# Kernel tuning notes

Hardware: AMD Instinct MI355X
Metric: run time of the kernel (lower is better)

Reference implementation:

```python
import jax, jax.numpy as jnp
import numpy as np
from jax import lax

BN_EPS = 1e-5

def _conv1d_same(x, w):
    # x: [N, 1, C], w: [1, 1, k] with k odd -> SAME padding along channel axis
    k = w.shape[-1]
    return lax.conv_general_dilated(x, w, window_strides=(1,),
                                    padding=[(k // 2, k // 2)],
                                    dimension_numbers=('NCH', 'OIH', 'NCH'))

def setup_inputs() -> dict:
    key = jax.random.key(0)
    ks = jax.random.split(key, 6)
    B, C, H, W = 4, 64, 64, 64
    kk = 3  # kernel size from in_dim=64: t=int(abs(log2(64)+1)/2)=3 (odd)
    x = jax.random.normal(ks[0], (B, C, H, W), dtype=jnp.float32)
    q_w = jax.random.normal(ks[1], (1, 1, kk), dtype=jnp.float32) * 0.5
    k_w = jax.random.normal(ks[2], (1, 1, kk), dtype=jnp.float32) * 0.5
    v_w = jax.random.normal(ks[3], (C, C), dtype=jnp.float32) * (1.0 / np.sqrt(C))
    v_b = jnp.zeros((C,), dtype=jnp.float32)
    gamma = jax.random.uniform(ks[4], (1,), dtype=jnp.float32, minval=0.5, maxval=1.5)
    bn_w = jnp.ones((C,), dtype=jnp.float32)
    bn_b = jnp.zeros((C,), dtype=jnp.float32)
    return {"x": x, "q_w": q_w, "k_w": k_w, "v_w": v_w, "v_b": v_b,
            "gamma": gamma, "bn_w": bn_w, "bn_b": bn_b}

def reference(x, q_w, k_w, v_w, v_b, gamma, bn_w, bn_b):
    B, C, H, W = x.shape
    N = H * W
    # conv1d Q/K projections over the channel axis, per spatial position
    xp = x.reshape(B, C, N).transpose(0, 2, 1).reshape(B * N, 1, C)
    q = _conv1d_same(xp, q_w).reshape(B, N, C)   # proj_query: [B, HW, C]
    k = _conv1d_same(xp, k_w).reshape(B, N, C)   # proj_key (pre-permute)
    energy = jnp.einsum('bnc,bmc->bnm', q, k)    # [B, HW, HW]
    attn = jax.nn.softmax(energy, axis=-1)
    # 1x1 value conv
    v = jnp.einsum('oc,bchw->bohw', v_w, x) + v_b[None, :, None, None]
    vv = v.reshape(B, C, N)
    # bmm(value, attention^T)
    out = jnp.einsum('bcm,bnm->bcn', vv, attn).reshape(B, C, H, W)
    y = gamma[0] * out
    # BatchNorm2d, training mode (batch statistics, biased variance)
    mean = jnp.mean(y, axis=(0, 2, 3), keepdims=True)
    var = jnp.var(y, axis=(0, 2, 3), keepdims=True)
    y = (y - mean) * lax.rsqrt(var + BN_EPS)
    y = y * bn_w[None, :, None, None] + bn_b[None, :, None, None]
    return y + x
```

## Files before the change

### kernel.cpp

```cpp
#include <hip/hip_runtime.h>
#include <stdint.h>

using f16 = _Float16;

typedef _Float16 f16x8 __attribute__((ext_vector_type(8)));
typedef _Float16 f16x4 __attribute__((ext_vector_type(4)));
typedef float f32x4 __attribute__((ext_vector_type(4)));

#define LOG2E 1.44269504088896340736f

__device__ __forceinline__ f16 f2h(float f) { return (f16)f; }

#if __has_builtin(__builtin_amdgcn_exp2f)
__device__ __forceinline__ float fexp2(float x) { return __builtin_amdgcn_exp2f(x); }
#else
__device__ __forceinline__ float fexp2(float x) { return exp2f(x); }
#endif

typedef __attribute__((address_space(1))) const uint32_t gu32;
typedef __attribute__((address_space(3))) uint32_t lu32;

__device__ __forceinline__ void dma16(const void* g, void* l) {
  __builtin_amdgcn_global_load_lds((gu32*)g, (lu32*)l, 16, 0, 0);
}

__device__ __forceinline__ f16x8 cvt8(const float* p) {
  const float4 a = *(const float4*)p;
  const float4 b = *(const float4*)(p + 4);
  f16x8 r;
  r[0] = (f16)a.x; r[1] = (f16)a.y; r[2] = (f16)a.z; r[3] = (f16)a.w;
  r[4] = (f16)b.x; r[5] = (f16)b.y; r[6] = (f16)b.z; r[7] = (f16)b.w;
  return r;
}


__global__ __launch_bounds__(256, 2) void pam_pre(
    const float* __restrict__ x, const float* __restrict__ qw,
    const float* __restrict__ kw, const float* __restrict__ vw,
    const float* __restrict__ vb,
    f16* __restrict__ qa, f16* __restrict__ ka2, f16* __restrict__ va3,
    float* __restrict__ gz)
{
  __shared__ alignas(16) f16 xt[16 * 72];
  const int tid = threadIdx.x;
  const int b = blockIdx.x >> 8;
  const int n0 = (blockIdx.x & 255) << 4;
  const int lane = tid & 63;
  const int wv = tid >> 6;
  const int quad = lane >> 4, l15 = lane & 15;

  if (blockIdx.x == 0 && tid < 128) gz[tid] = 0.f;

  {
    const int c = tid >> 2;
    const int j0 = (tid & 3) << 2;
    const float4 v0 = *(const float4*)(x + ((size_t)(b * 64 + c) << 12) + n0 + j0);
    xt[(j0 + 0) * 72 + c] = f2h(v0.x);
    xt[(j0 + 1) * 72 + c] = f2h(v0.y);
    xt[(j0 + 2) * 72 + c] = f2h(v0.z);
    xt[(j0 + 3) * 72 + c] = f2h(v0.w);
  }
  __syncthreads();

  const float qw0 = qw[0], qw1 = qw[1], qw2 = qw[2];
  const float kw0 = kw[0], kw1 = kw[1], kw2 = kw[2];
  for (int p = 0; p < 4; ++p) {
    const int c = lane;
    const int jr = (p << 2) + wv;
    const int n = n0 + jr;
    const float xm = (c > 0) ? (float)xt[jr * 72 + c - 1] : 0.f;
    const float x0 = (float)xt[jr * 72 + c];
    const float xp = (c < 63) ? (float)xt[jr * 72 + c + 1] : 0.f;
    const float qv = (qw0 * xm + qw1 * x0 + qw2 * xp) * LOG2E;
    const float kv = kw0 * xm + kw1 * x0 + kw2 * xp;
    qa[((size_t)((b << 12) + n) << 6) + c] = f2h(qv);
    ka2[((size_t)(b * 8 + (c >> 3)) << 15) + (n << 3) + (c & 7)] = f2h(kv);
  }

  {
    const f16x8 a0 = cvt8(vw + (wv * 16 + l15) * 64 + quad * 8);
    const f16x8 a1 = cvt8(vw + (wv * 16 + l15) * 64 + quad * 8 + 32);
    const f16x8 b0 = *(const f16x8*)&xt[l15 * 72 + quad * 8];
    const f16x8 b1 = *(const f16x8*)&xt[l15 * 72 + quad * 8 + 32];
    f32x4 z = {0.f, 0.f, 0.f, 0.f};
    z = __builtin_amdgcn_mfma_f32_16x16x32_f16(a0, b0, z, 0, 0, 0);
    z = __builtin_amdgcn_mfma_f32_16x16x32_f16(a1, b1, z, 0, 0, 0);
    const int cobase = wv * 16 + quad * 4;
    for (int r = 0; r < 4; ++r) {
      const int co = cobase + r;
      const int n = n0 + l15;
      const float val = z[r] + vb[co];
      va3[(((size_t)(b * 512 + (n >> 3))) << 9) + (co << 3) + (n & 7)] = f2h(val);
    }
  }
}

__global__ __launch_bounds__(512, 2) void pam_attn(
    const f16* __restrict__ qa, const f16* __restrict__ ka2,
    const f16* __restrict__ va3, const float* __restrict__ gam,
    float* __restrict__ y0, float* __restrict__ gs1, float* __restrict__ gs2)
{
  __shared__ alignas(16) f16 kbuf[2][8192];
  __shared__ alignas(16) f16 vbuf[2][8192];
  __shared__ float ldsO[32 * 65];
  __shared__ float ldsM[4][32], ldsL[4][32], ldsMg[32], ldsInv[32];

  const int tid = threadIdx.x;
  const int wv = tid >> 6, lane = tid & 63;
  const int quad = lane >> 4, l15 = lane & 15;
  const int ks = wv & 3, qh = wv >> 2;
  const int b = blockIdx.x & 3;
  const int qb = blockIdx.x >> 2;
  const int qb0 = qb << 5;
  const int phase = qb & 31;

  for (int i = tid; i < 32 * 65; i += 512) ldsO[i] = 0.f;

  const int bn = b << 12;
  f16x8 bq0, bq1;
  {
    const int q = qb0 + qh * 16 + l15;
    const f16* qp = qa + ((size_t)(bn + q) << 6) + quad * 8;
    bq0 = *(const f16x8*)qp;
    bq1 = *(const f16x8*)(qp + 32);
  }

  const f16* kg0 = ka2 + (((size_t)(b * 8 + wv)) << 15) + (lane << 3);
  const f16* vg0 = va3 + ((size_t)b << 18) + (wv << 10) + (lane << 3);

  f32x4 o[4] = {};
  float m = -1e30f, lp = 0.f;

  dma16(kg0 + ((size_t)phase << 10),       kbuf[0] + (wv << 10));
  dma16(kg0 + ((size_t)phase << 10) + 512, kbuf[0] + (wv << 10) + 512);
  dma16(vg0 + ((size_t)phase << 13),       vbuf[0] + (wv << 10));
  dma16(vg0 + ((size_t)phase << 13) + 512, vbuf[0] + (wv << 10) + 512);
  __syncthreads();

  const int kperm = (ks << 5) + (((l15 >> 2) << 3) | (l15 & 3));
  const int koff0 = kperm << 3;
  const int koff1 = (kperm + 4) << 3;
  const int vbase = ((ks * 4 + quad) << 9) + (l15 << 3);

#pragma unroll 1
  for (int kt = 0; kt < 32; ++kt) {
    const int cur = kt & 1;
    {
      const int tn = (kt + 1 + phase) & 31;
      f16* kd = kbuf[cur ^ 1] + (wv << 10);
      f16* vd = vbuf[cur ^ 1] + (wv << 10);
      dma16(kg0 + ((size_t)tn << 10),       kd);
      dma16(kg0 + ((size_t)tn << 10) + 512, kd + 512);
      dma16(vg0 + ((size_t)tn << 13),       vd);
      dma16(vg0 + ((size_t)tn << 13) + 512, vd + 512);
    }

    const f16* kc = kbuf[cur];
    const f16* vc = vbuf[cur];
    const f16x8 ak00 = *(const f16x8*)(kc + (quad << 10) + koff0);
    const f16x8 ak01 = *(const f16x8*)(kc + ((4 + quad) << 10) + koff0);
    const f16x8 ak10 = *(const f16x8*)(kc + (quad << 10) + koff1);
    const f16x8 ak11 = *(const f16x8*)(kc + ((4 + quad) << 10) + koff1);

    f32x4 z0, z1;
    {
      f32x4 z = {0.f, 0.f, 0.f, 0.f};
      z = __builtin_amdgcn_mfma_f32_16x16x32_f16(ak00, bq0, z, 0, 0, 0);
      z0 = __builtin_amdgcn_mfma_f32_16x16x32_f16(ak01, bq1, z, 0, 0, 0);
    }
    {
      f32x4 z = {0.f, 0.f, 0.f, 0.f};
      z = __builtin_amdgcn_mfma_f32_16x16x32_f16(ak10, bq0, z, 0, 0, 0);
      s1_label:
      z1 = __builtin_amdgcn_mfma_f32_16x16x32_f16(ak11, bq1, z, 0, 0, 0);
    }

    float tmax = fmaxf(fmaxf(fmaxf(z0[0], z0[1]), fmaxf(z0[2], z0[3])),
                       fmaxf(fmaxf(z1[0], z1[1]), fmaxf(z1[2], z1[3])));
    tmax = fmaxf(tmax, __shfl_xor(tmax, 16, 64));
    tmax = fmaxf(tmax, __shfl_xor(tmax, 32, 64));
    const bool need = !__all(tmax <= m + 8.f);
    const float mn = need ? fmaxf(m, tmax) : m;

    const float p0 = fexp2(z0[0] - mn);
    const float p1 = fexp2(z0[1] - mn);
    const float p2 = fexp2(z0[2] - mn);
    const float p3 = fexp2(z0[3] - mn);
    const float p4 = fexp2(z1[0] - mn);
    const float p5 = fexp2(z1[1] - mn);
    const float p6 = fexp2(z1[2] - mn);
    const float p7 = fexp2(z1[3] - mn);
    const float ts = ((p0 + p1) + (p2 + p3)) + ((p4 + p5) + (p6 + p7));

    f16x8 pa;
    pa[0] = f2h(p0); pa[1] = f2h(p1); pa[2] = f2h(p2); pa[3] = f2h(p3);
    pa[4] = f2h(p4); pa[5] = f2h(p5); pa[6] = f2h(p6); pa[7] = f2h(p7);

    if (need) {
      const float al = fexp2(m - mn);
      lp = lp * al + ts;
      m = mn;
#pragma unroll
      for (int ct = 0; ct < 4; ++ct)
        for (int r = 0; r < 4; ++r) o[ct][r] *= al;
    } else {
      lp += ts;
    }

#pragma unroll
    for (int ct = 0; ct < 4; ++ct) {
      const f16x8 av = *(const f16x8*)(vc + vbase + ct * 128);
      o[ct] = __builtin_amdgcn_mfma_f32_16x16x32_f16(av, pa, o[ct], 0, 0, 0);
    }
    __syncthreads();
  }

  {
    float v = lp;
    v += __shfl_xor(v, 16, 64);
    v += __shfl_xor(v, 32, 64);
    if (quad == 0) {
      ldsM[ks][qh * 16 + l15] = m;
      ldsL[ks][qh * 16 + l15] = v;
    }
  }
  __syncthreads();

  if (tid < 32) {
    const float M = fmaxf(fmaxf(ldsM[0][tid], ldsM[1][tid]),
                          fmaxf(ldsM[2][tid], ldsM[3][tid]));
    const float lt = ldsL[0][tid] * fexp2(ldsM[0][tid] - M) +
                     ldsL[1][tid] * fexp2(ldsM[1][tid] - M) +
                     ldsL[2][tid] * fexp2(ldsM[2][tid] - M) +
                     ldsL[3][tid] * fexp2(ldsM[3][tid] - M);
    ldsMg[tid] = M;
    ldsInv[tid] = 1.f / lt;
  }
  __syncthreads();

  {
    const int q = qh * 16 + l15;
    const float sc = fexp2(m - ldsMg[q]);
#pragma unroll
    for (int ct = 0; ct < 4; ++ct)
      for (int r = 0; r < 4; ++r)
        atomicAdd(&ldsO[q * 65 + ct * 16 + quad * 4 + r], o[ct][r] * sc);
  }
  __syncthreads();

  const float g = gam[0];
  {
    const int c = tid >> 3;
    const int q0 = (tid & 7) << 2;
    float4 v4;
    float* vp = &v4.x;
    float s1 = 0.f, s2 = 0.f;
    for (int r = 0; r < 4; ++r) {
      const float val = g * ldsO[(q0 + r) * 65 + c] * ldsInv[q0 + r];
      vp[r] = val; s1 += val; s2 += val * val;
    }
    *(float4*)(y0 + ((size_t)(b * 64 + c) << 12) + qb0 + q0) = v4;
    s1 += __shfl_xor(s1, 1, 64);
    s2 += __shfl_xor(s2, 1, 64);
    s1 += __shfl_xor(s1, 2, 64);
    s2 += __shfl_xor(s2, 2, 64);
    s1 += __shfl_xor(s1, 4, 64);
    s2 += __shfl_xor(s2, 4, 64);
    if ((tid & 7) == 0) {
      atomicAdd(&gs1[c], s1);
      atomicAdd(&gs2[c], s2);
    }
  }
}

__global__ __launch_bounds__(256, 2) void pam_apply(
    const float* __restrict__ y0, const float* __restrict__ x,
    const float* __restrict__ gs1, const float* __restrict__ gs2,
    const float* __restrict__ bnw, const float* __restrict__ bnb,
    float* __restrict__ out)
{
  const int i = (blockIdx.x * 256 + threadIdx.x) << 2;
  const int c = (i >> 12) & 63;
  const float inv_n = 1.f / 16384.f;
  const float mean = gs1[c] * inv_n;
  const float var = fmaxf(gs2[c] * inv_n - mean * mean, 0.f);
  const float sc = bnw[c] * rsqrtf(var + 1e-5f);
  const float sh = bnb[c] - mean * sc;
  const float4 y = *(const float4*)(y0 + i);
  const float4 xv = *(const float4*)(x + i);
  float4 r;
  r.x = y.x * sc + sh + xv.x;
  r.y = y.y * sc + sh + xv.y;
  r.z = y.z * sc + sh + xv.z;
  r.w = y.w * sc + sh + xv.w;
  *(float4*)(out + i) = r;
}

extern "C" void kernel_launch(void* const* d_in, const int* in_sizes, int n_in,
                              void* d_out, int out_size, void* d_ws, size_t ws_size,
                              hipStream_t stream)
{
  (void)in_sizes; (void)n_in; (void)out_size; (void)ws_size;
  const float* x   = (const float*)d_in[0];
  const float* qw  = (const float*)d_in[1];
  const float* kw  = (const float*)d_in[2];
  const float* vw  = (const float*)d_in[3];
  const float* vb  = (const float*)d_in[4];
  const float* gam = (const float*)d_in[5];
  const float* bnw = (const float*)d_in[6];
  const float* bnb = (const float*)d_in[7];

  char* ws = (char*)d_ws;
  f16*   qa  = (f16*)(ws);
  f16*   ka2 = (f16*)(ws + (2u << 20));
  f16*   va3 = (f16*)(ws + (4u << 20));
  float* y0  = (float*)(ws + (6u << 20));
  float* gs1 = (float*)(ws + (10u << 20));
  float* gs2 = (float*)(ws + (10u << 20) + 256);

  pam_pre  <<<1024, 256, 0, stream>>>(x, qw, kw, vw, vb, qa, ka2, va3, gs1);
  pam_attn <<<512, 512, 0, stream>>>(qa, ka2, va3, gam, y0, gs1, gs2);
  pam_apply<<<1024, 256, 0, stream>>>(y0, x, gs1, gs2, bnw, bnb, (float*)d_out);
}
```

Measured before the change: 149.7 us.

## Widen attention blocks to 64 queries and 1024 threads with swizzled K layout

The attention kernel now processes 64 queries per block using 16 waves, with 8 key splits and two query sub-tiles per wave. Each K/V tile loaded into LDS is therefore reused across twice as many queries, halving the grid and the total K/V traffic. Tiles are twice as large (128 keys) and staged in 128KB of dynamic LDS, which is aliased for the output reduction. The K layout written by the pre-kernel is XOR-swizzled to avoid LDS bank conflicts on the new read pattern. The cost is higher LDS and register pressure per block and only 256 blocks to spread across the GPU.

```diff
diff --git a/kernel.cpp b/kernel.cpp
--- a/kernel.cpp
+++ b/kernel.cpp
@@ -74,7 +74,8 @@
     const float qv = (qw0 * xm + qw1 * x0 + qw2 * xp) * LOG2E;
     const float kv = kw0 * xm + kw1 * x0 + kw2 * xp;
     qa[((size_t)((b << 12) + n) << 6) + c] = f2h(qv);
-    ka2[((size_t)(b * 8 + (c >> 3)) << 15) + (n << 3) + (c & 7)] = f2h(kv);
+    const int np = n ^ ((((n >> 3) & 1) << 2) | ((n >> 4) & 1));
+    ka2[((size_t)(b * 8 + (c >> 3)) << 15) + (np << 3) + (c & 7)] = f2h(kv);
   }
 
   {
@@ -95,166 +96,208 @@
   }
 }
 
-__global__ __launch_bounds__(512, 2) void pam_attn(
+__global__ __launch_bounds__(1024, 4) void pam_attn(
     const f16* __restrict__ qa, const f16* __restrict__ ka2,
     const f16* __restrict__ va3, const float* __restrict__ gam,
     float* __restrict__ y0, float* __restrict__ gs1, float* __restrict__ gs2)
 {
-  __shared__ alignas(16) f16 kbuf[2][8192];
-  __shared__ alignas(16) f16 vbuf[2][8192];
-  __shared__ float ldsO[32 * 65];
-  __shared__ float ldsM[4][32], ldsL[4][32], ldsMg[32], ldsInv[32];
+  extern __shared__ char smem[];
+  f16* const kbase = (f16*)smem;
+  f16* const vbase2 = (f16*)(smem + 65536);
+  float* const ldsO = (float*)smem;
+  __shared__ float ldsM[8][64], ldsL[8][64], ldsMg[64], ldsInv[64];
 
   const int tid = threadIdx.x;
   const int wv = tid >> 6, lane = tid & 63;
   const int quad = lane >> 4, l15 = lane & 15;
-  const int ks = wv & 3, qh = wv >> 2;
-  const int b = blockIdx.x & 3;
-  const int qb = blockIdx.x >> 2;
-  const int qb0 = qb << 5;
-  const int phase = qb & 31;
-
-  for (int i = tid; i < 32 * 65; i += 512) ldsO[i] = 0.f;
+  const int ks = wv & 7, qh = wv >> 3;
+  const int slot = (int)blockIdx.x & 7;
+  const int b = slot >> 1;
+  const int qb = (((int)blockIdx.x >> 3) << 1) | (slot & 1);
+  const int qb0 = qb << 6;
+  const int phase = qb & 15;
 
   const int bn = b << 12;
-  f16x8 bq0, bq1;
-  {
-    const int q = qb0 + qh * 16 + l15;
-    const f16* qp = qa + ((size_t)(bn + q) << 6) + quad * 8;
-    bq0 = *(const f16x8*)qp;
-    bq1 = *(const f16x8*)(qp + 32);
-  }
-
-  const f16* kg0 = ka2 + (((size_t)(b * 8 + wv)) << 15) + (lane << 3);
+  f16x8 bq00, bq01, bq10, bq11;
+  {
+    const f16* qp0 = qa + ((size_t)(bn + qb0 + qh * 32 + l15) << 6) + quad * 8;
+    bq00 = *(const f16x8*)qp0;
+    bq01 = *(const f16x8*)(qp0 + 32);
+    const f16* qp1 = qp0 + (16 << 6);
+    bq10 = *(const f16x8*)qp1;
+    bq11 = *(const f16x8*)(qp1 + 32);
+  }
+
+  const f16* kg0 = ka2 + (((size_t)(b * 8 + (wv >> 1))) << 15)
+                 + ((wv & 1) << 10) + (lane << 3);
   const f16* vg0 = va3 + ((size_t)b << 18) + (wv << 10) + (lane << 3);
 
-  f32x4 o[4] = {};
-  float m = -1e30f, lp = 0.f;
-
-  dma16(kg0 + ((size_t)phase << 10),       kbuf[0] + (wv << 10));
-  dma16(kg0 + ((size_t)phase << 10) + 512, kbuf[0] + (wv << 10) + 512);
-  dma16(vg0 + ((size_t)phase << 13),       vbuf[0] + (wv << 10));
-  dma16(vg0 + ((size_t)phase << 13) + 512, vbuf[0] + (wv << 10) + 512);
-  __syncthreads();
-
-  const int kperm = (ks << 5) + (((l15 >> 2) << 3) | (l15 & 3));
-  const int koff0 = kperm << 3;
-  const int koff1 = (kperm + 4) << 3;
+  f32x4 o0[4] = {}, o1[4] = {};
+  float m0 = -1e30f, lp0 = 0.f, m1 = -1e30f, lp1 = 0.f;
+
+  dma16(kg0 + ((size_t)phase << 11),       kbase + (wv << 10));
+  dma16(kg0 + ((size_t)phase << 11) + 512, kbase + (wv << 10) + 512);
+  dma16(vg0 + ((size_t)phase << 14),       vbase2 + (wv << 10));
+  dma16(vg0 + ((size_t)phase << 14) + 512, vbase2 + (wv << 10) + 512);
+  __syncthreads();
+
+  const int u = l15 >> 2;
+  const int xm = ((u & 1) << 2) | (u >> 1);
+  const int pos0 = (ks << 5) + (u << 3) + (l15 & 3);
+  const int koff0 = (pos0 ^ xm) << 3;
+  const int koff1 = koff0 ^ 32;
   const int vbase = ((ks * 4 + quad) << 9) + (l15 << 3);
 
 #pragma unroll 1
-  for (int kt = 0; kt < 32; ++kt) {
+  for (int kt = 0; kt < 16; ++kt) {
     const int cur = kt & 1;
-    {
-      const int tn = (kt + 1 + phase) & 31;
-      f16* kd = kbuf[cur ^ 1] + (wv << 10);
-      f16* vd = vbuf[cur ^ 1] + (wv << 10);
-      dma16(kg0 + ((size_t)tn << 10),       kd);
-      dma16(kg0 + ((size_t)tn << 10) + 512, kd + 512);
-      dma16(vg0 + ((size_t)tn << 13),       vd);
-      dma16(vg0 + ((size_t)tn << 13) + 512, vd + 512);
-    }
-
-    const f16* kc = kbuf[cur];
-    const f16* vc = vbuf[cur];
-    const f16x8 ak00 = *(const f16x8*)(kc + (quad << 10) + koff0);
-    const f16x8 ak01 = *(const f16x8*)(kc + ((4 + quad) << 10) + koff0);
-    const f16x8 ak10 = *(const f16x8*)(kc + (quad << 10) + koff1);
-    const f16x8 ak11 = *(const f16x8*)(kc + ((4 + quad) << 10) + koff1);
-
-    f32x4 z0, z1;
+    if (kt < 15) {
+      const int tn = (kt + 1 + phase) & 15;
+      f16* kd = kbase + ((cur ^ 1) << 14) + (wv << 10);
+      f16* vd = vbase2 + ((cur ^ 1) << 14) + (wv << 10);
+      dma16(kg0 + ((size_t)tn << 11),       kd);
+      dma16(kg0 + ((size_t)tn << 11) + 512, kd + 512);
+      dma16(vg0 + ((size_t)tn << 14),       vd);
+      dma16(vg0 + ((size_t)tn << 14) + 512, vd + 512);
+    }
+
+    const f16* kc = kbase + (cur << 14);
+    const f16* vc = vbase2 + (cur << 14);
+    const f16x8 ak00 = *(const f16x8*)(kc + (quad << 11) + koff0);
+    const f16x8 ak01 = *(const f16x8*)(kc + ((4 + quad) << 11) + koff0);
+    const f16x8 ak10 = *(const f16x8*)(kc + (quad << 11) + koff1);
+    const f16x8 ak11 = *(const f16x8*)(kc + ((4 + quad) << 11) + koff1);
+
+    f32x4 za0, zb0, za1, zb1;
     {
       f32x4 z = {0.f, 0.f, 0.f, 0.f};
-      z = __builtin_amdgcn_mfma_f32_16x16x32_f16(ak00, bq0, z, 0, 0, 0);
-      z0 = __builtin_amdgcn_mfma_f32_16x16x32_f16(ak01, bq1, z, 0, 0, 0);
+      z = __builtin_amdgcn_mfma_f32_16x16x32_f16(ak00, bq00, z, 0, 0, 0);
+      za0 = __builtin_amdgcn_mfma_f32_16x16x32_f16(ak01, bq01, z, 0, 0, 0);
     }
     {
       f32x4 z = {0.f, 0.f, 0.f, 0.f};
-      z = __builtin_amdgcn_mfma_f32_16x16x32_f16(ak10, bq0, z, 0, 0, 0);
-      s1_label:
-      z1 = __builtin_amdgcn_mfma_f32_16x16x32_f16(ak11, bq1, z, 0, 0, 0);
-    }
-
-    float tmax = fmaxf(fmaxf(fmaxf(z0[0], z0[1]), fmaxf(z0[2], z0[3])),
-                       fmaxf(fmaxf(z1[0], z1[1]), fmaxf(z1[2], z1[3])));
-    tmax = fmaxf(tmax, __shfl_xor(tmax, 16, 64));
-    tmax = fmaxf(tmax, __shfl_xor(tmax, 32, 64));
-    const bool need = !__all(tmax <= m + 8.f);
-    const float mn = need ? fmaxf(m, tmax) : m;
-
-    const float p0 = fexp2(z0[0] - mn);
-    const float p1 = fexp2(z0[1] - mn);
-    const float p2 = fexp2(z0[2] - mn);
-    const float p3 = fexp2(z0[3] - mn);
-    const float p4 = fexp2(z1[0] - mn);
-    const float p5 = fexp2(z1[1] - mn);
-    const float p6 = fexp2(z1[2] - mn);
-    const float p7 = fexp2(z1[3] - mn);
-    const float ts = ((p0 + p1) + (p2 + p3)) + ((p4 + p5) + (p6 + p7));
-
-    f16x8 pa;
-    pa[0] = f2h(p0); pa[1] = f2h(p1); pa[2] = f2h(p2); pa[3] = f2h(p3);
-    pa[4] = f2h(p4); pa[5] = f2h(p5); pa[6] = f2h(p6); pa[7] = f2h(p7);
-
-    if (need) {
-      const float al = fexp2(m - mn);
-      lp = lp * al + ts;
-      m = mn;
-#pragma unroll
-      for (int ct = 0; ct < 4; ++ct)
-        for (int r = 0; r < 4; ++r) o[ct][r] *= al;
-    } else {
-      lp += ts;
+      z = __builtin_amdgcn_mfma_f32_16x16x32_f16(ak10, bq00, z, 0, 0, 0);
+      zb0 = __builtin_amdgcn_mfma_f32_16x16x32_f16(ak11, bq01, z, 0, 0, 0);
+    }
+    {
+      f32x4 z = {0.f, 0.f, 0.f, 0.f};
+      z = __builtin_amdgcn_mfma_f32_16x16x32_f16(ak00, bq10, z, 0, 0, 0);
+      za1 = __builtin_amdgcn_mfma_f32_16x16x32_f16(ak01, bq11, z, 0, 0, 0);
+    }
+    {
+      f32x4 z = {0.f, 0.f, 0.f, 0.f};
+      z = __builtin_amdgcn_mfma_f32_16x16x32_f16(ak10, bq10, z, 0, 0, 0);
+      zb1 = __builtin_amdgcn_mfma_f32_16x16x32_f16(ak11, bq11, z, 0, 0, 0);
+    }
+
+    f16x8 pa0, pa1;
+    {
+      float tmax = fmaxf(fmaxf(fmaxf(za0[0], za0[1]), fmaxf(za0[2], za0[3])),
+                         fmaxf(fmaxf(zb0[0], zb0[1]), fmaxf(zb0[2], zb0[3])));
+      tmax = fmaxf(tmax, __shfl_xor(tmax, 16, 64));
+      tmax = fmaxf(tmax, __shfl_xor(tmax, 32, 64));
+      const bool need = !__all(tmax <= m0 + 8.f);
+      const float mn = need ? fmaxf(m0, tmax) : m0;
+      const float p0 = fexp2(za0[0] - mn), p1 = fexp2(za0[1] - mn);
+      const float p2 = fexp2(za0[2] - mn), p3 = fexp2(za0[3] - mn);
+      const float p4 = fexp2(zb0[0] - mn), p5 = fexp2(zb0[1] - mn);
+      const float p6 = fexp2(zb0[2] - mn), p7 = fexp2(zb0[3] - mn);
+      const float ts = ((p0 + p1) + (p2 + p3)) + ((p4 + p5) + (p6 + p7));
+      pa0[0] = f2h(p0); pa0[1] = f2h(p1); pa0[2] = f2h(p2); pa0[3] = f2h(p3);
+      pa0[4] = f2h(p4); pa0[5] = f2h(p5); pa0[6] = f2h(p6); pa0[7] = f2h(p7);
+      if (need) {
+        const float al = fexp2(m0 - mn);
+        lp0 = lp0 * al + ts;
+        m0 = mn;
+#pragma unroll
+        for (int ct = 0; ct < 4; ++ct)
+          for (int r = 0; r < 4; ++r) o0[ct][r] *= al;
+      } else {
+        lp0 += ts;
+      }
+    }
+    {
+      float tmax = fmaxf(fmaxf(fmaxf(za1[0], za1[1]), fmaxf(za1[2], za1[3])),
+                         fmaxf(fmaxf(zb1[0], zb1[1]), fmaxf(zb1[2], zb1[3])));
+      tmax = fmaxf(tmax, __shfl_xor(tmax, 16, 64));
+      tmax = fmaxf(tmax, __shfl_xor(tmax, 32, 64));
+      const bool need = !__all(tmax <= m1 + 8.f);
+      const float mn = need ? fmaxf(m1, tmax) : m1;
+      const float p0 = fexp2(za1[0] - mn), p1 = fexp2(za1[1] - mn);
+      const float p2 = fexp2(za1[2] - mn), p3 = fexp2(za1[3] - mn);
+      const float p4 = fexp2(zb1[0] - mn), p5 = fexp2(zb1[1] - mn);
+      const float p6 = fexp2(zb1[2] - mn), p7 = fexp2(zb1[3] - mn);
+      const float ts = ((p0 + p1) + (p2 + p3)) + ((p4 + p5) + (p6 + p7));
+      pa1[0] = f2h(p0); pa1[1] = f2h(p1); pa1[2] = f2h(p2); pa1[3] = f2h(p3);
+      pa1[4] = f2h(p4); pa1[5] = f2h(p5); pa1[6] = f2h(p6); pa1[7] = f2h(p7);
+      if (need) {
+        const float al = fexp2(m1 - mn);
+        lp1 = lp1 * al + ts;
+        m1 = mn;
+#pragma unroll
+        for (int ct = 0; ct < 4; ++ct)
+          for (int r = 0; r < 4; ++r) o1[ct][r] *= al;
+      } else {
+        lp1 += ts;
+      }
     }
 
 #pragma unroll
     for (int ct = 0; ct < 4; ++ct) {
       const f16x8 av = *(const f16x8*)(vc + vbase + ct * 128);
-      o[ct] = __builtin_amdgcn_mfma_f32_16x16x32_f16(av, pa, o[ct], 0, 0, 0);
+      o0[ct] = __builtin_amdgcn_mfma_f32_16x16x32_f16(av, pa0, o0[ct], 0, 0, 0);
+      o1[ct] = __builtin_amdgcn_mfma_f32_16x16x32_f16(av, pa1, o1[ct], 0, 0, 0);
     }
     __syncthreads();
   }
 
-  {
-    float v = lp;
-    v += __shfl_xor(v, 16, 64);
-    v += __shfl_xor(v, 32, 64);
-    if (quad == 0) {
-      ldsM[ks][qh * 16 + l15] = m;
-      ldsL[ks][qh * 16 + l15] = v;
-    }
-  }
-  __syncthreads();
-
-  if (tid < 32) {
-    const float M = fmaxf(fmaxf(ldsM[0][tid], ldsM[1][tid]),
-                          fmaxf(ldsM[2][tid], ldsM[3][tid]));
-    const float lt = ldsL[0][tid] * fexp2(ldsM[0][tid] - M) +
-                     ldsL[1][tid] * fexp2(ldsM[1][tid] - M) +
-                     ldsL[2][tid] * fexp2(ldsM[2][tid] - M) +
-                     ldsL[3][tid] * fexp2(ldsM[3][tid] - M);
+  lp0 += __shfl_xor(lp0, 16, 64);
+  lp0 += __shfl_xor(lp0, 32, 64);
+  lp1 += __shfl_xor(lp1, 16, 64);
+  lp1 += __shfl_xor(lp1, 32, 64);
+  if (quad == 0) {
+    ldsM[ks][qh * 32 + l15] = m0;
+    ldsL[ks][qh * 32 + l15] = lp0;
+    ldsM[ks][qh * 32 + 16 + l15] = m1;
+    ldsL[ks][qh * 32 + 16 + l15] = lp1;
+  }
+  __syncthreads();
+
+  for (int i = tid; i < 64 * 65; i += 1024) ldsO[i] = 0.f;
+  if (tid < 64) {
+    float M = ldsM[0][tid];
+#pragma unroll
+    for (int k = 1; k < 8; ++k) M = fmaxf(M, ldsM[k][tid]);
+    float lt = 0.f;
+#pragma unroll
+    for (int k = 0; k < 8; ++k) lt += ldsL[k][tid] * fexp2(ldsM[k][tid] - M);
     ldsMg[tid] = M;
     ldsInv[tid] = 1.f / lt;
   }
   __syncthreads();
 
   {
-    const int q = qh * 16 + l15;
-    const float sc = fexp2(m - ldsMg[q]);
+    const int q0i = qh * 32 + l15, q1i = q0i + 16;
+    const float sc0 = fexp2(m0 - ldsMg[q0i]);
+    const float sc1 = fexp2(m1 - ldsMg[q1i]);
 #pragma unroll
     for (int ct = 0; ct < 4; ++ct)
-      for (int r = 0; r < 4; ++r)
-        atomicAdd(&ldsO[q * 65 + ct * 16 + quad * 4 + r], o[ct][r] * sc);
+      for (int r = 0; r < 4; ++r) {
+        const int c = ct * 16 + quad * 4 + r;
+        atomicAdd(&ldsO[q0i * 65 + c], o0[ct][r] * sc0);
+        atomicAdd(&ldsO[q1i * 65 + c], o1[ct][r] * sc1);
+      }
   }
   __syncthreads();
 
   const float g = gam[0];
   {
-    const int c = tid >> 3;
-    const int q0 = (tid & 7) << 2;
+    const int c = tid >> 4;
+    const int q0 = (tid & 15) << 2;
     float4 v4;
     float* vp = &v4.x;
     float s1 = 0.f, s2 = 0.f;
+#pragma unroll
     for (int r = 0; r < 4; ++r) {
       const float val = g * ldsO[(q0 + r) * 65 + c] * ldsInv[q0 + r];
       vp[r] = val; s1 += val; s2 += val * val;
@@ -266,7 +309,9 @@
     s2 += __shfl_xor(s2, 2, 64);
     s1 += __shfl_xor(s1, 4, 64);
     s2 += __shfl_xor(s2, 4, 64);
-    if ((tid & 7) == 0) {
+    s1 += __shfl_xor(s1, 8, 64);
+    s2 += __shfl_xor(s2, 8, 64);
+    if ((tid & 15) == 0) {
       atomicAdd(&gs1[c], s1);
       atomicAdd(&gs2[c], s2);
     }
@@ -318,7 +363,14 @@
   float* gs1 = (float*)(ws + (10u << 20));
   float* gs2 = (float*)(ws + (10u << 20) + 256);
 
+  static bool lds_init = false;
+  if (!lds_init) {
+    (void)hipFuncSetAttribute((const void*)pam_attn,
+                              hipFuncAttributeMaxDynamicSharedMemorySize, 131072);
+    lds_init = true;
+  }
+
   pam_pre  <<<1024, 256, 0, stream>>>(x, qw, kw, vw, vb, qa, ka2, va3, gs1);
-  pam_attn <<<512, 512, 0, stream>>>(qa, ka2, va3, gam, y0, gs1, gs2);
+  pam_attn <<<256, 1024, 131072, stream>>>(qa, ka2, va3, gam, y0, gs1, gs2);
   pam_apply<<<1024, 256, 0, stream>>>(y0, x, gs1, gs2, bnw, bnb, (float*)d_out);
 }
```

Measured after the change: 176.6 us. 17.9% more time.

## Use 4-slot LDS ring with 64-key tiles and lighter barriers in attention

Applied to the files above, without the earlier changes.

Splits the key loop into 64 smaller tiles of 64 keys each and streams K/V into a 4-slot dynamic-LDS ring that prefetches two tiles ahead. The full __syncthreads is replaced by an explicit vmcnt wait plus s_barrier, so only the oldest loads are drained. The PV product switches to 16x16x16 MFMA with f16x4 operands. The output accumulation buffer now aliases the K region of the ring. The aim is to hide global-to-LDS latency and shrink per-iteration stalls, at the cost of twice as many loop iterations and softmax reductions, and the aliasing must not race with in-flight DMA.

```diff
diff --git a/kernel.cpp b/kernel.cpp
--- a/kernel.cpp
+++ b/kernel.cpp
@@ -100,9 +100,10 @@
     const f16* __restrict__ va3, const float* __restrict__ gam,
     float* __restrict__ y0, float* __restrict__ gs1, float* __restrict__ gs2)
 {
-  __shared__ alignas(16) f16 kbuf[2][8192];
-  __shared__ alignas(16) f16 vbuf[2][8192];
-  __shared__ float ldsO[32 * 65];
+  extern __shared__ char smem[];
+  f16* const kbase = (f16*)smem;
+  f16* const vbase = (f16*)(smem + 32768);
+  float* const ldsO = (float*)smem;
   __shared__ float ldsM[4][32], ldsL[4][32], ldsMg[32], ldsInv[32];
 
   const int tid = threadIdx.x;
@@ -112,9 +113,7 @@
   const int b = blockIdx.x & 3;
   const int qb = blockIdx.x >> 2;
   const int qb0 = qb << 5;
-  const int phase = qb & 31;
-
-  for (int i = tid; i < 32 * 65; i += 512) ldsO[i] = 0.f;
+  const int phase = qb & 63;
 
   const int bn = b << 12;
   f16x8 bq0, bq1;
@@ -126,75 +125,61 @@
   }
 
   const f16* kg0 = ka2 + (((size_t)(b * 8 + wv)) << 15) + (lane << 3);
-  const f16* vg0 = va3 + ((size_t)b << 18) + (wv << 10) + (lane << 3);
+  const f16* vg0 = va3 + ((size_t)b << 18) + (wv << 9) + (lane << 3);
 
   f32x4 o[4] = {};
   float m = -1e30f, lp = 0.f;
 
-  dma16(kg0 + ((size_t)phase << 10),       kbuf[0] + (wv << 10));
-  dma16(kg0 + ((size_t)phase << 10) + 512, kbuf[0] + (wv << 10) + 512);
-  dma16(vg0 + ((size_t)phase << 13),       vbuf[0] + (wv << 10));
-  dma16(vg0 + ((size_t)phase << 13) + 512, vbuf[0] + (wv << 10) + 512);
-  __syncthreads();
-
-  const int kperm = (ks << 5) + (((l15 >> 2) << 3) | (l15 & 3));
-  const int koff0 = kperm << 3;
-  const int koff1 = (kperm + 4) << 3;
-  const int vbase = ((ks * 4 + quad) << 9) + (l15 << 3);
+  {
+    const int g0 = phase;
+    const int g1 = (1 + phase) & 63;
+    dma16(kg0 + ((size_t)g0 << 9),  kbase + (wv << 9));
+    dma16(vg0 + ((size_t)g0 << 12), vbase + (wv << 9));
+    dma16(kg0 + ((size_t)g1 << 9),  kbase + 4096 + (wv << 9));
+    dma16(vg0 + ((size_t)g1 << 12), vbase + 4096 + (wv << 9));
+  }
+  asm volatile("s_waitcnt vmcnt(2)" ::: "memory");
+  __builtin_amdgcn_s_barrier();
+
+  const int krow = ((ks << 4) + l15) << 3;
+  const int vrow = ((ks * 2 + (quad >> 1)) << 9) + ((quad & 1) << 2);
 
 #pragma unroll 1
-  for (int kt = 0; kt < 32; ++kt) {
-    const int cur = kt & 1;
+  for (int kt = 0; kt < 64; ++kt) {
+    const int slot = kt & 3;
     {
-      const int tn = (kt + 1 + phase) & 31;
-      f16* kd = kbuf[cur ^ 1] + (wv << 10);
-      f16* vd = vbuf[cur ^ 1] + (wv << 10);
-      dma16(kg0 + ((size_t)tn << 10),       kd);
-      dma16(kg0 + ((size_t)tn << 10) + 512, kd + 512);
-      dma16(vg0 + ((size_t)tn << 13),       vd);
-      dma16(vg0 + ((size_t)tn << 13) + 512, vd + 512);
-    }
-
-    const f16* kc = kbuf[cur];
-    const f16* vc = vbuf[cur];
-    const f16x8 ak00 = *(const f16x8*)(kc + (quad << 10) + koff0);
-    const f16x8 ak01 = *(const f16x8*)(kc + ((4 + quad) << 10) + koff0);
-    const f16x8 ak10 = *(const f16x8*)(kc + (quad << 10) + koff1);
-    const f16x8 ak11 = *(const f16x8*)(kc + ((4 + quad) << 10) + koff1);
-
-    f32x4 z0, z1;
+      const int g = (kt + 2 + phase) & 63;
+      const int ps = ((kt + 2) & 3) << 12;
+      dma16(kg0 + ((size_t)g << 9),  kbase + ps + (wv << 9));
+      dma16(vg0 + ((size_t)g << 12), vbase + ps + (wv << 9));
+    }
+
+    const f16* kc = kbase + (slot << 12);
+    const f16* vc = vbase + (slot << 12);
+    const f16x8 ak0 = *(const f16x8*)(kc + (quad << 9) + krow);
+    const f16x8 ak1 = *(const f16x8*)(kc + ((4 + quad) << 9) + krow);
+
+    f32x4 z;
     {
-      f32x4 z = {0.f, 0.f, 0.f, 0.f};
-      z = __builtin_amdgcn_mfma_f32_16x16x32_f16(ak00, bq0, z, 0, 0, 0);
-      z0 = __builtin_amdgcn_mfma_f32_16x16x32_f16(ak01, bq1, z, 0, 0, 0);
-    }
-    {
-      f32x4 z = {0.f, 0.f, 0.f, 0.f};
-      z = __builtin_amdgcn_mfma_f32_16x16x32_f16(ak10, bq0, z, 0, 0, 0);
-      s1_label:
-      z1 = __builtin_amdgcn_mfma_f32_16x16x32_f16(ak11, bq1, z, 0, 0, 0);
-    }
-
-    float tmax = fmaxf(fmaxf(fmaxf(z0[0], z0[1]), fmaxf(z0[2], z0[3])),
-                       fmaxf(fmaxf(z1[0], z1[1]), fmaxf(z1[2], z1[3])));
+      f32x4 zz = {0.f, 0.f, 0.f, 0.f};
+      zz = __builtin_amdgcn_mfma_f32_16x16x32_f16(ak0, bq0, zz, 0, 0, 0);
+      z  = __builtin_amdgcn_mfma_f32_16x16x32_f16(ak1, bq1, zz, 0, 0, 0);
+    }
+
+    float tmax = fmaxf(fmaxf(z[0], z[1]), fmaxf(z[2], z[3]));
     tmax = fmaxf(tmax, __shfl_xor(tmax, 16, 64));
     tmax = fmaxf(tmax, __shfl_xor(tmax, 32, 64));
     const bool need = !__all(tmax <= m + 8.f);
     const float mn = need ? fmaxf(m, tmax) : m;
 
-    const float p0 = fexp2(z0[0] - mn);
-    const float p1 = fexp2(z0[1] - mn);
-    const float p2 = fexp2(z0[2] - mn);
-    const float p3 = fexp2(z0[3] - mn);
-    const float p4 = fexp2(z1[0] - mn);
-    const float p5 = fexp2(z1[1] - mn);
-    const float p6 = fexp2(z1[2] - mn);
-    const float p7 = fexp2(z1[3] - mn);
-    const float ts = ((p0 + p1) + (p2 + p3)) + ((p4 + p5) + (p6 + p7));
-
-    f16x8 pa;
+    const float p0 = fexp2(z[0] - mn);
+    const float p1 = fexp2(z[1] - mn);
+    const float p2 = fexp2(z[2] - mn);
+    const float p3 = fexp2(z[3] - mn);
+    const float ts = (p0 + p1) + (p2 + p3);
+
+    f16x4 pa;
     pa[0] = f2h(p0); pa[1] = f2h(p1); pa[2] = f2h(p2); pa[3] = f2h(p3);
-    pa[4] = f2h(p4); pa[5] = f2h(p5); pa[6] = f2h(p6); pa[7] = f2h(p7);
 
     if (need) {
       const float al = fexp2(m - mn);
@@ -209,23 +194,25 @@
 
 #pragma unroll
     for (int ct = 0; ct < 4; ++ct) {
-      const f16x8 av = *(const f16x8*)(vc + vbase + ct * 128);
-      o[ct] = __builtin_amdgcn_mfma_f32_16x16x32_f16(av, pa, o[ct], 0, 0, 0);
-    }
-    __syncthreads();
-  }
-
-  {
-    float v = lp;
-    v += __shfl_xor(v, 16, 64);
-    v += __shfl_xor(v, 32, 64);
-    if (quad == 0) {
-      ldsM[ks][qh * 16 + l15] = m;
-      ldsL[ks][qh * 16 + l15] = v;
-    }
+      const f16x4 av = *(const f16x4*)(vc + vrow + ((ct * 16 + l15) << 3));
+      o[ct] = __builtin_amdgcn_mfma_f32_16x16x16f16(av, pa, o[ct], 0, 0, 0);
+    }
+
+    asm volatile("s_waitcnt vmcnt(2)" ::: "memory");
+    __builtin_amdgcn_s_barrier();
+  }
+
+  asm volatile("s_waitcnt vmcnt(0)" ::: "memory");
+
+  lp += __shfl_xor(lp, 16, 64);
+  lp += __shfl_xor(lp, 32, 64);
+  if (quad == 0) {
+    ldsM[ks][qh * 16 + l15] = m;
+    ldsL[ks][qh * 16 + l15] = lp;
   }
   __syncthreads();
 
+  for (int i = tid; i < 32 * 65; i += 512) ldsO[i] = 0.f;
   if (tid < 32) {
     const float M = fmaxf(fmaxf(ldsM[0][tid], ldsM[1][tid]),
                           fmaxf(ldsM[2][tid], ldsM[3][tid]));
@@ -318,7 +305,14 @@
   float* gs1 = (float*)(ws + (10u << 20));
   float* gs2 = (float*)(ws + (10u << 20) + 256);
 
+  static bool lds_init = false;
+  if (!lds_init) {
+    (void)hipFuncSetAttribute((const void*)pam_attn,
+                              hipFuncAttributeMaxDynamicSharedMemorySize, 65536);
+    lds_init = true;
+  }
+
   pam_pre  <<<1024, 256, 0, stream>>>(x, qw, kw, vw, vb, qa, ka2, va3, gs1);
-  pam_attn <<<512, 512, 0, stream>>>(qa, ka2, va3, gam, y0, gs1, gs2);
+  pam_attn <<<512, 512, 65536, stream>>>(qa, ka2, va3, gam, y0, gs1, gs2);
   pam_apply<<<1024, 256, 0, stream>>>(y0, x, gs1, gs2, bnw, bnb, (float*)d_out);
 }
```

After: 161.1 us. +7.6%, slower.

## Widen pre-pass tiles, vectorize Q/K/V stores, and XOR-swizzle K layout

Applied to the files above, without the earlier changes.

The pre-pass kernel now handles 64 spatial positions per block instead of 16, cutting the grid from 1024 to 256 blocks. Q and K are computed eight channels per thread and written with 16-byte vector stores. The V projection is restructured so each wave reuses its x fragment across four output-channel tiles, writing f16x4 vectors. K is stored with an XOR permutation of position indices, and the attention kernel's K offsets are recomputed to match; the likely aim is to reduce LDS bank conflicts or simplify addressing. The pre-pass is a small share of total time, so most of the expected change comes from the K-read pattern in the attention loop.

```diff
diff --git a/kernel.cpp b/kernel.cpp
--- a/kernel.cpp
+++ b/kernel.cpp
@@ -41,10 +41,10 @@
     f16* __restrict__ qa, f16* __restrict__ ka2, f16* __restrict__ va3,
     float* __restrict__ gz)
 {
-  __shared__ alignas(16) f16 xt[16 * 72];
+  __shared__ alignas(16) f16 xt[64 * 72];
   const int tid = threadIdx.x;
-  const int b = blockIdx.x >> 8;
-  const int n0 = (blockIdx.x & 255) << 4;
+  const int b = blockIdx.x >> 6;
+  const int n0 = (blockIdx.x & 63) << 6;
   const int lane = tid & 63;
   const int wv = tid >> 6;
   const int quad = lane >> 4, l15 = lane & 15;
@@ -53,44 +53,62 @@
 
   {
     const int c = tid >> 2;
-    const int j0 = (tid & 3) << 2;
-    const float4 v0 = *(const float4*)(x + ((size_t)(b * 64 + c) << 12) + n0 + j0);
-    xt[(j0 + 0) * 72 + c] = f2h(v0.x);
-    xt[(j0 + 1) * 72 + c] = f2h(v0.y);
-    xt[(j0 + 2) * 72 + c] = f2h(v0.z);
-    xt[(j0 + 3) * 72 + c] = f2h(v0.w);
+    const int j0 = (tid & 3) << 4;
+    const float* xp = x + ((size_t)(b * 64 + c) << 12) + n0 + j0;
+#pragma unroll
+    for (int j = 0; j < 4; ++j) {
+      const float4 v0 = *(const float4*)(xp + j * 4);
+      const int n = j0 + j * 4;
+      xt[(n + 0) * 72 + c] = f2h(v0.x);
+      xt[(n + 1) * 72 + c] = f2h(v0.y);
+      xt[(n + 2) * 72 + c] = f2h(v0.z);
+      xt[(n + 3) * 72 + c] = f2h(v0.w);
+    }
   }
   __syncthreads();
 
   const float qw0 = qw[0], qw1 = qw[1], qw2 = qw[2];
   const float kw0 = kw[0], kw1 = kw[1], kw2 = kw[2];
-  for (int p = 0; p < 4; ++p) {
-    const int c = lane;
-    const int jr = (p << 2) + wv;
-    const int n = n0 + jr;
-    const float xm = (c > 0) ? (float)xt[jr * 72 + c - 1] : 0.f;
-    const float x0 = (float)xt[jr * 72 + c];
-    const float xp = (c < 63) ? (float)xt[jr * 72 + c + 1] : 0.f;
-    const float qv = (qw0 * xm + qw1 * x0 + qw2 * xp) * LOG2E;
-    const float kv = kw0 * xm + kw1 * x0 + kw2 * xp;
-    qa[((size_t)((b << 12) + n) << 6) + c] = f2h(qv);
-    ka2[((size_t)(b * 8 + (c >> 3)) << 15) + (n << 3) + (c & 7)] = f2h(kv);
-  }
-
-  {
-    const f16x8 a0 = cvt8(vw + (wv * 16 + l15) * 64 + quad * 8);
-    const f16x8 a1 = cvt8(vw + (wv * 16 + l15) * 64 + quad * 8 + 32);
-    const f16x8 b0 = *(const f16x8*)&xt[l15 * 72 + quad * 8];
-    const f16x8 b1 = *(const f16x8*)&xt[l15 * 72 + quad * 8 + 32];
-    f32x4 z = {0.f, 0.f, 0.f, 0.f};
-    z = __builtin_amdgcn_mfma_f32_16x16x32_f16(a0, b0, z, 0, 0, 0);
-    z = __builtin_amdgcn_mfma_f32_16x16x32_f16(a1, b1, z, 0, 0, 0);
-    const int cobase = wv * 16 + quad * 4;
-    for (int r = 0; r < 4; ++r) {
-      const int co = cobase + r;
-      const int n = n0 + l15;
-      const float val = z[r] + vb[co];
-      va3[(((size_t)(b * 512 + (n >> 3))) << 9) + (co << 3) + (n & 7)] = f2h(val);
+#pragma unroll
+  for (int i = 0; i < 2; ++i) {
+    const int n = (tid >> 3) + i * 32;
+    const int c8 = tid & 7;
+    const f16x8 v0 = *(const f16x8*)&xt[n * 72 + c8 * 8];
+    const float lm = (c8 > 0) ? (float)xt[n * 72 + c8 * 8 - 1] : 0.f;
+    const float rp = (c8 < 7) ? (float)xt[n * 72 + c8 * 8 + 8] : 0.f;
+    f16x8 qv8, kv8;
+#pragma unroll
+    for (int j = 0; j < 8; ++j) {
+      const float xm = (j == 0) ? lm : (float)v0[j - 1];
+      const float x0 = (float)v0[j];
+      const float xp = (j == 7) ? rp : (float)v0[j + 1];
+      qv8[j] = f2h((qw0 * xm + qw1 * x0 + qw2 * xp) * LOG2E);
+      kv8[j] = f2h(kw0 * xm + kw1 * x0 + kw2 * xp);
+    }
+    const int nn = n0 + n;
+    *(f16x8*)(qa + ((size_t)((b << 12) + nn) << 6) + c8 * 8) = qv8;
+    const int np = nn ^ ((((nn >> 3) & 1) << 2) | ((nn >> 4) & 1));
+    *(f16x8*)(ka2 + (((size_t)(b * 8 + c8)) << 15) + (np << 3)) = kv8;
+  }
+
+  {
+    const f16x8 a0 = *(const f16x8*)&xt[(wv * 16 + l15) * 72 + quad * 8];
+    const f16x8 a1 = *(const f16x8*)&xt[(wv * 16 + l15) * 72 + quad * 8 + 32];
+    const int nb = n0 + wv * 16 + quad * 4;
+#pragma unroll
+    for (int ct = 0; ct < 4; ++ct) {
+      const int co = ct * 16 + l15;
+      const f16x8 b0 = cvt8(vw + co * 64 + quad * 8);
+      const f16x8 b1 = cvt8(vw + co * 64 + quad * 8 + 32);
+      f32x4 z = {0.f, 0.f, 0.f, 0.f};
+      z = __builtin_amdgcn_mfma_f32_16x16x32_f16(a0, b0, z, 0, 0, 0);
+      z = __builtin_amdgcn_mfma_f32_16x16x32_f16(a1, b1, z, 0, 0, 0);
+      const float vbv = vb[co];
+      f16x4 pv;
+#pragma unroll
+      for (int r = 0; r < 4; ++r) pv[r] = f2h(z[r] + vbv);
+      *(f16x4*)(va3 + (((size_t)(b * 512 + (nb >> 3))) << 9)
+                + (co << 3) + (nb & 7)) = pv;
     }
   }
 }
@@ -137,9 +155,11 @@
   dma16(vg0 + ((size_t)phase << 13) + 512, vbuf[0] + (wv << 10) + 512);
   __syncthreads();
 
-  const int kperm = (ks << 5) + (((l15 >> 2) << 3) | (l15 & 3));
-  const int koff0 = kperm << 3;
-  const int koff1 = (kperm + 4) << 3;
+  const int u = l15 >> 2;
+  const int xmsk = ((u & 1) << 2) | (u >> 1);
+  const int pos0 = (ks << 5) + (u << 3) + (l15 & 3);
+  const int koff0 = (pos0 ^ xmsk) << 3;
+  const int koff1 = koff0 ^ 32;
   const int vbase = ((ks * 4 + quad) << 9) + (l15 << 3);
 
 #pragma unroll 1
@@ -171,7 +191,6 @@
     {
       f32x4 z = {0.f, 0.f, 0.f, 0.f};
       z = __builtin_amdgcn_mfma_f32_16x16x32_f16(ak10, bq0, z, 0, 0, 0);
-      s1_label:
       z1 = __builtin_amdgcn_mfma_f32_16x16x32_f16(ak11, bq1, z, 0, 0, 0);
     }
 
@@ -318,7 +337,7 @@
   float* gs1 = (float*)(ws + (10u << 20));
   float* gs2 = (float*)(ws + (10u << 20) + 256);
 
-  pam_pre  <<<1024, 256, 0, stream>>>(x, qw, kw, vw, vb, qa, ka2, va3, gs1);
+  pam_pre  <<<256, 256, 0, stream>>>(x, qw, kw, vw, vb, qa, ka2, va3, gs1);
   pam_attn <<<512, 512, 0, stream>>>(qa, ka2, va3, gam, y0, gs1, gs2);
   pam_apply<<<1024, 256, 0, stream>>>(y0, x, gs1, gs2, bnw, bnb, (float*)d_out);
 }
```

Result: no change. 147.2 us (-1.7%).
